# Kernel optimization log

Hardware: AMD Instinct MI355X
Metric: run time of the kernel (lower is better)

## Reference

```python
import jax, jax.numpy as jnp
import numpy as np

MARGIN = 0.3
FAMILY_TABLE = jnp.array([0, 1, 2, 1, 3, 3], dtype=jnp.int32)  # num_classes == 6
_BIG = 1e9  # finite sentinel (avoids inf*0 NaNs under autodiff)
_EPS = 1e-12  # F.normalize eps


def setup_inputs() -> dict:
    key = jax.random.key(0)
    k1, k2 = jax.random.split(key)
    B, D = 8192, 64
    embeddings = jax.random.normal(k1, (B, D), dtype=jnp.float32)
    labels = jax.random.randint(k2, (B,), 0, 6, dtype=jnp.int64)
    return {"embeddings": embeddings, "labels": labels}


def reference(embeddings, labels):
    B = embeddings.shape[0]
    # fam[i] = family_table[labels[i]]; labels are always < len(table) here,
    # so no -1 entries occur (matches original semantics for in-range labels).
    fam = jnp.take(FAMILY_TABLE, labels)  # [B]

    # L2-normalize rows (F.normalize with eps clamp)
    norm = jnp.maximum(jnp.linalg.norm(embeddings, axis=-1, keepdims=True), _EPS)
    emb_norm = embeddings / norm

    # cosine distance matrix [B, B]
    dist = 1.0 - emb_norm @ emb_norm.T

    same = (fam[:, None] == fam[None, :]) & (~jnp.eye(B, dtype=bool))  # [B,B]
    diff = fam[:, None] != fam[None, :]                                 # [B,B]

    d_pos = jnp.max(jnp.where(same, dist, -_BIG), axis=1)  # hardest positive
    d_neg = jnp.min(jnp.where(diff, dist, _BIG), axis=1)   # hardest negative

    valid = same.any(axis=1) & diff.any(axis=1)  # rows contributing to loss
    per_row = jnp.where(valid, jax.nn.relu(d_pos - d_neg + MARGIN), 0.0)

    count = jnp.sum(valid.astype(jnp.float32))
    return jnp.sum(per_row) / jnp.maximum(count, 1.0)
```

## Files before the change

### kernel.cpp

```cpp
#include <hip/hip_runtime.h>
#include <math.h>

#define MARGIN 0.3f
#define NJ 32
#define NPAIR 8

typedef short bf16x8 __attribute__((ext_vector_type(8)));
typedef float f32x4 __attribute__((ext_vector_type(4)));
typedef unsigned int u32;
typedef const __attribute__((address_space(1))) u32* gp_t;
typedef __attribute__((address_space(3))) u32* lp_t;

__device__ __forceinline__ unsigned short f2bf_rne(float x) {
    unsigned b = __float_as_uint(x);
    unsigned r = b + 0x7FFFu + ((b >> 16) & 1u);
    return (unsigned short)(r >> 16);
}
__device__ __forceinline__ int fam_of(int lbl) { return (0xF64 >> (2 * lbl)) & 3; }

__global__ __launch_bounds__(1024) void sort_kernel(const int* __restrict__ labels,
                                                    int* __restrict__ posOf,
                                                    unsigned char* __restrict__ famSorted,
                                                    int* __restrict__ famLoHi,
                                                    unsigned* __restrict__ counter, int B) {
    const int t = threadIdx.x;
    const int lane = t & 63, w = t >> 6;
    if (t == 0) *counter = 0;
    int lc[4] = {0, 0, 0, 0};
    int lf[8], lr[8];
#pragma unroll
    for (int j = 0; j < 8; j++) {
        int f = fam_of(labels[t * 8 + j]);
        lf[j] = f; lr[j] = lc[f]++;
    }
    int inc[4];
#pragma unroll
    for (int f = 0; f < 4; f++) {
        int v = lc[f];
#pragma unroll
        for (int o = 1; o < 64; o <<= 1) {
            int u = __shfl_up(v, o, 64);
            if (lane >= o) v += u;
        }
        inc[f] = v;
    }
    __shared__ int waveTot[16][4], waveBase[16][4], famBase[4], famTotS[4];
    if (lane == 63)
#pragma unroll
        for (int f = 0; f < 4; f++) waveTot[w][f] = inc[f];
    __syncthreads();
    if (t < 64) {
        int f = t >> 4, ww = t & 15;
        int v = waveTot[ww][f];
#pragma unroll
        for (int o = 1; o < 16; o <<= 1) {
            int u = __shfl_up(v, o, 64);
            if ((t & 15) >= o) v += u;
        }
        waveBase[ww][f] = v - waveTot[ww][f];
        if (ww == 15) famTotS[f] = v;
    }
    __syncthreads();
    if (t == 0) {
        int b = 0;
#pragma unroll
        for (int f = 0; f < 4; f++) {
            famBase[f] = b; famLoHi[f] = b; b += famTotS[f]; famLoHi[4 + f] = b;
        }
    }
    __syncthreads();
    int base[4];
#pragma unroll
    for (int f = 0; f < 4; f++) base[f] = famBase[f] + waveBase[w][f] + (inc[f] - lc[f]);
#pragma unroll
    for (int j = 0; j < 8; j++) {
        int pos = base[lf[j]] + lr[j];
        posOf[t * 8 + j] = pos;
        famSorted[pos] = (unsigned char)lf[j];
    }
}

__global__ __launch_bounds__(256) void normpack_kernel(const float* __restrict__ emb,
                                                       const int* __restrict__ posOf,
                                                       short* __restrict__ pack, int B) {
    const int lane = threadIdx.x & 63;
    const int wid  = threadIdx.x >> 6;
    const int row  = blockIdx.x * 4 + wid;
    float x = emb[(size_t)row * 64 + lane];
    float ss = x * x;
#pragma unroll
    for (int o = 32; o > 0; o >>= 1) ss += __shfl_xor(ss, o, 64);
    float n = fmaxf(sqrtf(ss), 1e-12f);
    unsigned short h = f2bf_rne(x / n);
    int pos = posOf[row];
    size_t idx = (size_t)(pos >> 4) * 1024 + (size_t)(lane >> 3) * 128 + (size_t)(pos & 15) * 8 + (lane & 7);
    pack[idx] = (short)h;
}

__global__ __launch_bounds__(256) void gemm_minmax_kernel(
    const short* __restrict__ pack,
    const unsigned char* __restrict__ famSorted, const int* __restrict__ famLoHi,
    float* __restrict__ pMin, float* __restrict__ pMax, int B) {
    __shared__ short ldsB[16384];

    const int lane = threadIdx.x & 63;
    const int wid  = threadIdx.x >> 6;
    const int g = lane >> 4;
    const int c = lane & 15;
    const int rowBase = blockIdx.x * 256 + wid * 64;
    const int aStrip0 = rowBase >> 4;
    const int jChunk0 = blockIdx.y * 256;
    const int jStrip0 = jChunk0 >> 4;

    bf16x8 aH[4][2];
#pragma unroll
    for (int s = 0; s < 4; s++) {
        const short* pA = pack + (size_t)(aStrip0 + s) * 1024;
        aH[s][0] = *(const bf16x8*)(pA + lane * 8);
        aH[s][1] = *(const bf16x8*)(pA + 512 + lane * 8);
    }

    {
        const char* src = (const char*)(pack + (size_t)jStrip0 * 1024);
#pragma unroll
        for (int i = 0; i < 8; i++) {
            int off = wid * 8192 + i * 1024;
            __builtin_amdgcn_global_load_lds((gp_t)(src + off + lane * 16),
                                             (lp_t)((char*)ldsB + off), 16, 0, 0);
        }
    }

    int sLo[4], sHi[4], sUni[4];
#pragma unroll
    for (int s = 0; s < 4; s++) {
        int f0  = famSorted[rowBase + s * 16];
        int f15 = famSorted[rowBase + s * 16 + 15];
        sUni[s] = __builtin_amdgcn_readfirstlane((f0 == f15) ? 1 : 0);
        sLo[s]  = __builtin_amdgcn_readfirstlane(famLoHi[f0]);
        sHi[s]  = __builtin_amdgcn_readfirstlane(famLoHi[4 + f0]);
    }

    const f32x4 zq = {0.f, 0.f, 0.f, 0.f};
    float mn[4] = {1e30f, 1e30f, 1e30f, 1e30f};
    float mx[4] = {-1e30f, -1e30f, -1e30f, -1e30f};

    __syncthreads();

#pragma unroll
    for (int jp = 0; jp < NPAIR; jp++) {
        const int j0 = jChunk0 + jp * 32;
        const short* pB0 = ldsB + (size_t)(2 * jp) * 1024;
        const short* pB1 = pB0 + 1024;
        bf16x8 b0h0 = *(const bf16x8*)(pB0 + lane * 8);
        bf16x8 b0h1 = *(const bf16x8*)(pB0 + 512 + lane * 8);
        bf16x8 b1h0 = *(const bf16x8*)(pB1 + lane * 8);
        bf16x8 b1h1 = *(const bf16x8*)(pB1 + 512 + lane * 8);

#pragma unroll
        for (int s = 0; s < 4; s++) {
            f32x4 accA, accB;
            accA = __builtin_amdgcn_mfma_f32_16x16x32_bf16(b0h0, aH[s][0], zq, 0, 0, 0);
            accB = __builtin_amdgcn_mfma_f32_16x16x32_bf16(b1h0, aH[s][0], zq, 0, 0, 0);
            accA = __builtin_amdgcn_mfma_f32_16x16x32_bf16(b0h1, aH[s][1], accA, 0, 0, 0);
            accB = __builtin_amdgcn_mfma_f32_16x16x32_bf16(b1h1, aH[s][1], accB, 0, 0, 0);

            if (sUni[s] && j0 >= sLo[s] && j0 + 32 <= sHi[s]) {
                float a01 = fminf(accA[0], accA[1]), a23 = fminf(accA[2], accA[3]);
                float b01 = fminf(accB[0], accB[1]), b23 = fminf(accB[2], accB[3]);
                mn[s] = fminf(mn[s], fminf(fminf(a01, a23), fminf(b01, b23)));
            } else if (sUni[s] && (j0 >= sHi[s] || j0 + 32 <= sLo[s])) {
                float a01 = fmaxf(accA[0], accA[1]), a23 = fmaxf(accA[2], accA[3]);
                float b01 = fmaxf(accB[0], accB[1]), b23 = fmaxf(accB[2], accB[3]);
                mx[s] = fmaxf(mx[s], fmaxf(fmaxf(a01, a23), fmaxf(b01, b23)));
            } else {
                int fi = famSorted[rowBase + s * 16 + c];
                unsigned fjA = *(const unsigned*)(famSorted + j0 + g * 4);
                unsigned fjB = *(const unsigned*)(famSorted + j0 + 16 + g * 4);
#pragma unroll
                for (int r = 0; r < 4; r++) {
                    bool sameA = ((int)((fjA >> (8 * r)) & 255u) == fi);
                    bool sameB = ((int)((fjB >> (8 * r)) & 255u) == fi);
                    mn[s] = fminf(mn[s], sameA ? accA[r] : 1e30f);
                    mx[s] = fmaxf(mx[s], sameA ? -1e30f : accA[r]);
                    mn[s] = fminf(mn[s], sameB ? accB[r] : 1e30f);
                    mx[s] = fmaxf(mx[s], sameB ? -1e30f : accB[r]);
                }
            }
        }
    }

#pragma unroll
    for (int s = 0; s < 4; s++) {
        float mnv = mn[s], mxv = mx[s];
        mnv = fminf(mnv, __shfl_xor(mnv, 16, 64));
        mxv = fmaxf(mxv, __shfl_xor(mxv, 16, 64));
        mnv = fminf(mnv, __shfl_xor(mnv, 32, 64));
        mxv = fmaxf(mxv, __shfl_xor(mxv, 32, 64));
        if (g == 0) {
            int row = rowBase + s * 16 + c;
            pMin[(size_t)blockIdx.y * B + row] = mnv;
            pMax[(size_t)blockIdx.y * B + row] = mxv;
        }
    }
}

__global__ __launch_bounds__(256) void rowloss_final_kernel(const float* __restrict__ pMin,
                                                            const float* __restrict__ pMax,
                                                            float* __restrict__ partial,
                                                            unsigned* __restrict__ counter,
                                                            float* __restrict__ out, int B) {
    const int nb = B / 256;
    const int row = blockIdx.x * 256 + threadIdx.x;
    float mn = 1e30f, mx = -1e30f;
#pragma unroll 8
    for (int cn = 0; cn < NJ; cn++) {
        mn = fminf(mn, pMin[(size_t)cn * B + row]);
        mx = fmaxf(mx, pMax[(size_t)cn * B + row]);
    }
    float sum = 0.f, cnt = 0.f;
    if (mn < 1e29f && mx > -1e29f) {
        sum = fmaxf(mx - mn + MARGIN, 0.f);
        cnt = 1.f;
    }
#pragma unroll
    for (int o = 32; o > 0; o >>= 1) {
        sum += __shfl_xor(sum, o, 64);
        cnt += __shfl_xor(cnt, o, 64);
    }
    __shared__ float sS[4], sC[4];
    const int lane = threadIdx.x & 63, w = threadIdx.x >> 6;
    if (lane == 0) { sS[w] = sum; sC[w] = cnt; }
    __syncthreads();
    if (threadIdx.x == 0) {
        partial[blockIdx.x]      = sS[0] + sS[1] + sS[2] + sS[3];
        partial[64 + blockIdx.x] = sC[0] + sC[1] + sC[2] + sC[3];
        __threadfence();
        unsigned done = atomicAdd(counter, 1u);
        if (done == (unsigned)(nb - 1)) {
            __threadfence();
            float S = 0.f, C = 0.f;
            for (int i = 0; i < nb; i++) { S += partial[i]; C += partial[64 + i]; }
            out[0] = S / fmaxf(C, 1.f);
        }
    }
}

extern "C" void kernel_launch(void* const* d_in, const int* in_sizes, int n_in,
                              void* d_out, int out_size, void* d_ws, size_t ws_size,
                              hipStream_t stream) {
    const float* emb    = (const float*)d_in[0];
    const int*   labels = (const int*)d_in[1];
    const int B = in_sizes[1];

    char* base = (char*)d_ws;
    size_t off = 0;
    auto alloc = [&](size_t bytes) -> char* {
        char* p = base + off;
        off = (off + bytes + 255) & ~(size_t)255;
        return p;
    };
    int*           posOf     = (int*)alloc((size_t)B * 4);
    unsigned char* famSorted = (unsigned char*)alloc((size_t)B);
    int*           famLoHi   = (int*)alloc(32);
    unsigned*      counter   = (unsigned*)alloc(64);
    short*         pack      = (short*)alloc((size_t)B * 64 * 2);
    float*         pMin      = (float*)alloc((size_t)NJ * B * 4);
    float*         pMax      = (float*)alloc((size_t)NJ * B * 4);
    float*         partial   = (float*)alloc(128 * 4);

    sort_kernel<<<1, 1024, 0, stream>>>(labels, posOf, famSorted, famLoHi, counter, B);
    normpack_kernel<<<B / 4, 256, 0, stream>>>(emb, posOf, pack, B);
    dim3 g3(B / 256, NJ);
    gemm_minmax_kernel<<<g3, 256, 0, stream>>>(pack, famSorted, famLoHi, pMin, pMax, B);
    rowloss_final_kernel<<<B / 256, 256, 0, stream>>>(pMin, pMax, partial, counter,
                                                      (float*)d_out, B);
}
```

Measured before the change: 33.26 us.

## Switch to 32x32 MFMA tiles and fuse row-loss reduction into GEMM tail

Repacks normalized embeddings into 32-row strips so the GEMM can use 32x32x16 bf16 MFMA, with each wave covering 128 rows against 256 columns. The separate row-loss kernel is folded into the GEMM: the last 32 blocks to finish spin until all 512 blocks have written their partial min/max, then reduce rows and compute the final loss. This removes a kernel launch and uses larger MFMA tiles, at the cost of higher register pressure and a spin-wait that relies on every block being resident or finishing.

```diff
diff --git a/kernel.cpp b/kernel.cpp
--- a/kernel.cpp
+++ b/kernel.cpp
@@ -2,11 +2,9 @@
 #include <math.h>
 
 #define MARGIN 0.3f
-#define NJ 32
-#define NPAIR 8
 
 typedef short bf16x8 __attribute__((ext_vector_type(8)));
-typedef float f32x4 __attribute__((ext_vector_type(4)));
+typedef float f32x16 __attribute__((ext_vector_type(16)));
 typedef unsigned int u32;
 typedef const __attribute__((address_space(1))) u32* gp_t;
 typedef __attribute__((address_space(3))) u32* lp_t;
@@ -22,10 +20,10 @@
                                                     int* __restrict__ posOf,
                                                     unsigned char* __restrict__ famSorted,
                                                     int* __restrict__ famLoHi,
-                                                    unsigned* __restrict__ counter, int B) {
+                                                    unsigned* __restrict__ counters, int B) {
     const int t = threadIdx.x;
     const int lane = t & 63, w = t >> 6;
-    if (t == 0) *counter = 0;
+    if (t < 2) counters[t] = 0;
     int lc[4] = {0, 0, 0, 0};
     int lf[8], lr[8];
 #pragma unroll
@@ -93,35 +91,40 @@
     float n = fmaxf(sqrtf(ss), 1e-12f);
     unsigned short h = f2bf_rne(x / n);
     int pos = posOf[row];
-    size_t idx = (size_t)(pos >> 4) * 1024 + (size_t)(lane >> 3) * 128 + (size_t)(pos & 15) * 8 + (lane & 7);
+    size_t idx = (size_t)(pos >> 5) * 2048 + (size_t)(lane >> 4) * 512 +
+                 (size_t)((lane >> 3) & 1) * 256 + (size_t)(pos & 31) * 8 + (lane & 7);
     pack[idx] = (short)h;
 }
 
-__global__ __launch_bounds__(256) void gemm_minmax_kernel(
+__global__ __launch_bounds__(256, 2) void gemm_tail_kernel(
     const short* __restrict__ pack,
     const unsigned char* __restrict__ famSorted, const int* __restrict__ famLoHi,
-    float* __restrict__ pMin, float* __restrict__ pMax, int B) {
+    float* __restrict__ pMin, float* __restrict__ pMax,
+    unsigned* __restrict__ counters, float* __restrict__ partial,
+    float* __restrict__ out, int B) {
     __shared__ short ldsB[16384];
-
-    const int lane = threadIdx.x & 63;
-    const int wid  = threadIdx.x >> 6;
-    const int g = lane >> 4;
-    const int c = lane & 15;
-    const int rowBase = blockIdx.x * 256 + wid * 64;
-    const int aStrip0 = rowBase >> 4;
-    const int jChunk0 = blockIdx.y * 256;
-    const int jStrip0 = jChunk0 >> 4;
-
-    bf16x8 aH[4][2];
+    const int t    = threadIdx.x;
+    const int lane = t & 63;
+    const int wid  = t >> 6;
+    const int half = lane >> 5;
+    const int il   = lane & 31;
+    const int rowBlock = blockIdx.x & 15;
+    const int colBlock = blockIdx.x >> 4;
+    const int rowBase  = rowBlock * 512 + wid * 128;
+    const int aStrip0  = rowBase >> 5;
+    const int jChunk0  = colBlock * 256;
+    const int jStrip0  = jChunk0 >> 5;
+
+    bf16x8 aH[4][4];
 #pragma unroll
     for (int s = 0; s < 4; s++) {
-        const short* pA = pack + (size_t)(aStrip0 + s) * 1024;
-        aH[s][0] = *(const bf16x8*)(pA + lane * 8);
-        aH[s][1] = *(const bf16x8*)(pA + 512 + lane * 8);
-    }
-
+        const short* pA = pack + (size_t)(aStrip0 + s) * 2048;
+#pragma unroll
+        for (int kw = 0; kw < 4; kw++)
+            aH[s][kw] = *(const bf16x8*)(pA + kw * 512 + lane * 8);
+    }
     {
-        const char* src = (const char*)(pack + (size_t)jStrip0 * 1024);
+        const char* src = (const char*)(pack + (size_t)jStrip0 * 2048);
 #pragma unroll
         for (int i = 0; i < 8; i++) {
             int off = wid * 8192 + i * 1024;
@@ -129,57 +132,64 @@
                                              (lp_t)((char*)ldsB + off), 16, 0, 0);
         }
     }
-
     int sLo[4], sHi[4], sUni[4];
 #pragma unroll
     for (int s = 0; s < 4; s++) {
-        int f0  = famSorted[rowBase + s * 16];
-        int f15 = famSorted[rowBase + s * 16 + 15];
-        sUni[s] = __builtin_amdgcn_readfirstlane((f0 == f15) ? 1 : 0);
+        int f0  = famSorted[rowBase + s * 32];
+        int f31 = famSorted[rowBase + s * 32 + 31];
+        sUni[s] = __builtin_amdgcn_readfirstlane((f0 == f31) ? 1 : 0);
         sLo[s]  = __builtin_amdgcn_readfirstlane(famLoHi[f0]);
         sHi[s]  = __builtin_amdgcn_readfirstlane(famLoHi[4 + f0]);
     }
-
-    const f32x4 zq = {0.f, 0.f, 0.f, 0.f};
+    const f32x16 zq = {0.f};
     float mn[4] = {1e30f, 1e30f, 1e30f, 1e30f};
     float mx[4] = {-1e30f, -1e30f, -1e30f, -1e30f};
 
     __syncthreads();
 
 #pragma unroll
-    for (int jp = 0; jp < NPAIR; jp++) {
-        const int j0 = jChunk0 + jp * 32;
-        const short* pB0 = ldsB + (size_t)(2 * jp) * 1024;
-        const short* pB1 = pB0 + 1024;
-        bf16x8 b0h0 = *(const bf16x8*)(pB0 + lane * 8);
-        bf16x8 b0h1 = *(const bf16x8*)(pB0 + 512 + lane * 8);
-        bf16x8 b1h0 = *(const bf16x8*)(pB1 + lane * 8);
-        bf16x8 b1h1 = *(const bf16x8*)(pB1 + 512 + lane * 8);
-
+    for (int pr = 0; pr < 4; pr++) {
+        const int j0 = jChunk0 + pr * 64;
+        const short* pB0 = ldsB + pr * 4096;
+        const short* pB1 = pB0 + 2048;
+        bf16x8 bA[4], bB[4];
+#pragma unroll
+        for (int kw = 0; kw < 4; kw++) {
+            bA[kw] = *(const bf16x8*)(pB0 + kw * 512 + lane * 8);
+            bB[kw] = *(const bf16x8*)(pB1 + kw * 512 + lane * 8);
+        }
 #pragma unroll
         for (int s = 0; s < 4; s++) {
-            f32x4 accA, accB;
-            accA = __builtin_amdgcn_mfma_f32_16x16x32_bf16(b0h0, aH[s][0], zq, 0, 0, 0);
-            accB = __builtin_amdgcn_mfma_f32_16x16x32_bf16(b1h0, aH[s][0], zq, 0, 0, 0);
-            accA = __builtin_amdgcn_mfma_f32_16x16x32_bf16(b0h1, aH[s][1], accA, 0, 0, 0);
-            accB = __builtin_amdgcn_mfma_f32_16x16x32_bf16(b1h1, aH[s][1], accB, 0, 0, 0);
-
-            if (sUni[s] && j0 >= sLo[s] && j0 + 32 <= sHi[s]) {
-                float a01 = fminf(accA[0], accA[1]), a23 = fminf(accA[2], accA[3]);
-                float b01 = fminf(accB[0], accB[1]), b23 = fminf(accB[2], accB[3]);
-                mn[s] = fminf(mn[s], fminf(fminf(a01, a23), fminf(b01, b23)));
-            } else if (sUni[s] && (j0 >= sHi[s] || j0 + 32 <= sLo[s])) {
-                float a01 = fmaxf(accA[0], accA[1]), a23 = fmaxf(accA[2], accA[3]);
-                float b01 = fmaxf(accB[0], accB[1]), b23 = fmaxf(accB[2], accB[3]);
-                mx[s] = fmaxf(mx[s], fmaxf(fmaxf(a01, a23), fmaxf(b01, b23)));
+            f32x16 accA = __builtin_amdgcn_mfma_f32_32x32x16_bf16(bA[0], aH[s][0], zq, 0, 0, 0);
+            f32x16 accB = __builtin_amdgcn_mfma_f32_32x32x16_bf16(bB[0], aH[s][0], zq, 0, 0, 0);
+            accA = __builtin_amdgcn_mfma_f32_32x32x16_bf16(bA[1], aH[s][1], accA, 0, 0, 0);
+            accB = __builtin_amdgcn_mfma_f32_32x32x16_bf16(bB[1], aH[s][1], accB, 0, 0, 0);
+            accA = __builtin_amdgcn_mfma_f32_32x32x16_bf16(bA[2], aH[s][2], accA, 0, 0, 0);
+            accB = __builtin_amdgcn_mfma_f32_32x32x16_bf16(bB[2], aH[s][2], accB, 0, 0, 0);
+            accA = __builtin_amdgcn_mfma_f32_32x32x16_bf16(bA[3], aH[s][3], accA, 0, 0, 0);
+            accB = __builtin_amdgcn_mfma_f32_32x32x16_bf16(bB[3], aH[s][3], accB, 0, 0, 0);
+
+            if (sUni[s] && j0 >= sLo[s] && j0 + 64 <= sHi[s]) {
+#pragma unroll
+                for (int r = 0; r < 16; r++)
+                    mn[s] = fminf(fminf(mn[s], accA[r]), accB[r]);
+            } else if (sUni[s] && (j0 >= sHi[s] || j0 + 64 <= sLo[s])) {
+#pragma unroll
+                for (int r = 0; r < 16; r++)
+                    mx[s] = fmaxf(fmaxf(mx[s], accA[r]), accB[r]);
             } else {
-                int fi = famSorted[rowBase + s * 16 + c];
-                unsigned fjA = *(const unsigned*)(famSorted + j0 + g * 4);
-                unsigned fjB = *(const unsigned*)(famSorted + j0 + 16 + g * 4);
-#pragma unroll
-                for (int r = 0; r < 4; r++) {
-                    bool sameA = ((int)((fjA >> (8 * r)) & 255u) == fi);
-                    bool sameB = ((int)((fjB >> (8 * r)) & 255u) == fi);
+                int fi = famSorted[rowBase + s * 32 + il];
+                u32 wA[4], wB[4];
+#pragma unroll
+                for (int q = 0; q < 4; q++) {
+                    wA[q] = *(const u32*)(famSorted + j0 + q * 8 + 4 * half);
+                    wB[q] = *(const u32*)(famSorted + j0 + 32 + q * 8 + 4 * half);
+                }
+#pragma unroll
+                for (int r = 0; r < 16; r++) {
+                    int fjA = (int)((wA[r >> 2] >> ((r & 3) * 8)) & 255u);
+                    int fjB = (int)((wB[r >> 2] >> ((r & 3) * 8)) & 255u);
+                    bool sameA = (fjA == fi), sameB = (fjB == fi);
                     mn[s] = fminf(mn[s], sameA ? accA[r] : 1e30f);
                     mx[s] = fmaxf(mx[s], sameA ? -1e30f : accA[r]);
                     mn[s] = fminf(mn[s], sameB ? accB[r] : 1e30f);
@@ -191,56 +201,56 @@
 
 #pragma unroll
     for (int s = 0; s < 4; s++) {
-        float mnv = mn[s], mxv = mx[s];
-        mnv = fminf(mnv, __shfl_xor(mnv, 16, 64));
-        mxv = fmaxf(mxv, __shfl_xor(mxv, 16, 64));
-        mnv = fminf(mnv, __shfl_xor(mnv, 32, 64));
-        mxv = fmaxf(mxv, __shfl_xor(mxv, 32, 64));
-        if (g == 0) {
-            int row = rowBase + s * 16 + c;
-            pMin[(size_t)blockIdx.y * B + row] = mnv;
-            pMax[(size_t)blockIdx.y * B + row] = mxv;
-        }
-    }
-}
-
-__global__ __launch_bounds__(256) void rowloss_final_kernel(const float* __restrict__ pMin,
-                                                            const float* __restrict__ pMax,
-                                                            float* __restrict__ partial,
-                                                            unsigned* __restrict__ counter,
-                                                            float* __restrict__ out, int B) {
-    const int nb = B / 256;
-    const int row = blockIdx.x * 256 + threadIdx.x;
-    float mn = 1e30f, mx = -1e30f;
+        float mnv = fminf(mn[s], __shfl_xor(mn[s], 32, 64));
+        float mxv = fmaxf(mx[s], __shfl_xor(mx[s], 32, 64));
+        if (half == 0) {
+            int row = rowBase + s * 32 + il;
+            pMin[(size_t)colBlock * B + row] = mnv;
+            pMax[(size_t)colBlock * B + row] = mxv;
+        }
+    }
+
+    __threadfence();
+    __shared__ unsigned sDone;
+    if (t == 0) sDone = atomicAdd(&counters[0], 1u);
+    __syncthreads();
+    unsigned done = sDone;
+    if (done >= 480u) {
+        if (t == 0) { while (atomicAdd(&counters[0], 0u) < 512u) {} }
+        __syncthreads();
+        __threadfence();
+        int slice = (int)done - 480;
+        int row = slice * 256 + t;
+        float rmn = 1e30f, rmx = -1e30f;
 #pragma unroll 8
-    for (int cn = 0; cn < NJ; cn++) {
-        mn = fminf(mn, pMin[(size_t)cn * B + row]);
-        mx = fmaxf(mx, pMax[(size_t)cn * B + row]);
-    }
-    float sum = 0.f, cnt = 0.f;
-    if (mn < 1e29f && mx > -1e29f) {
-        sum = fmaxf(mx - mn + MARGIN, 0.f);
-        cnt = 1.f;
-    }
-#pragma unroll
-    for (int o = 32; o > 0; o >>= 1) {
-        sum += __shfl_xor(sum, o, 64);
-        cnt += __shfl_xor(cnt, o, 64);
-    }
-    __shared__ float sS[4], sC[4];
-    const int lane = threadIdx.x & 63, w = threadIdx.x >> 6;
-    if (lane == 0) { sS[w] = sum; sC[w] = cnt; }
-    __syncthreads();
-    if (threadIdx.x == 0) {
-        partial[blockIdx.x]      = sS[0] + sS[1] + sS[2] + sS[3];
-        partial[64 + blockIdx.x] = sC[0] + sC[1] + sC[2] + sC[3];
-        __threadfence();
-        unsigned done = atomicAdd(counter, 1u);
-        if (done == (unsigned)(nb - 1)) {
+        for (int cn = 0; cn < 32; cn++) {
+            rmn = fminf(rmn, pMin[(size_t)cn * B + row]);
+            rmx = fmaxf(rmx, pMax[(size_t)cn * B + row]);
+        }
+        float sum = 0.f, cnt = 0.f;
+        if (rmn < 1e29f && rmx > -1e29f) {
+            sum = fmaxf(rmx - rmn + MARGIN, 0.f);
+            cnt = 1.f;
+        }
+#pragma unroll
+        for (int o = 32; o > 0; o >>= 1) {
+            sum += __shfl_xor(sum, o, 64);
+            cnt += __shfl_xor(cnt, o, 64);
+        }
+        __shared__ float sS[4], sC[4];
+        if (lane == 0) { sS[wid] = sum; sC[wid] = cnt; }
+        __syncthreads();
+        if (t == 0) {
+            partial[slice]      = sS[0] + sS[1] + sS[2] + sS[3];
+            partial[64 + slice] = sC[0] + sC[1] + sC[2] + sC[3];
             __threadfence();
-            float S = 0.f, C = 0.f;
-            for (int i = 0; i < nb; i++) { S += partial[i]; C += partial[64 + i]; }
-            out[0] = S / fmaxf(C, 1.f);
+            unsigned d2 = atomicAdd(&counters[1], 1u);
+            if (d2 == 31u) {
+                __threadfence();
+                float S = 0.f, C = 0.f;
+                for (int i = 0; i < 32; i++) { S += partial[i]; C += partial[64 + i]; }
+                out[0] = S / fmaxf(C, 1.f);
+            }
         }
     }
 }
@@ -261,17 +271,15 @@
     };
     int*           posOf     = (int*)alloc((size_t)B * 4);
     unsigned char* famSorted = (unsigned char*)alloc((size_t)B);
-    int*           famLoHi   = (int*)alloc(32);
-    unsigned*      counter   = (unsigned*)alloc(64);
+    int*           famLoHi   = (int*)alloc(64);
+    unsigned*      counters  = (unsigned*)alloc(64);
     short*         pack      = (short*)alloc((size_t)B * 64 * 2);
-    float*         pMin      = (float*)alloc((size_t)NJ * B * 4);
-    float*         pMax      = (float*)alloc((size_t)NJ * B * 4);
+    float*         pMin      = (float*)alloc((size_t)32 * B * 4);
+    float*         pMax      = (float*)alloc((size_t)32 * B * 4);
     float*         partial   = (float*)alloc(128 * 4);
 
-    sort_kernel<<<1, 1024, 0, stream>>>(labels, posOf, famSorted, famLoHi, counter, B);
+    sort_kernel<<<1, 1024, 0, stream>>>(labels, posOf, famSorted, famLoHi, counters, B);
     normpack_kernel<<<B / 4, 256, 0, stream>>>(emb, posOf, pack, B);
-    dim3 g3(B / 256, NJ);
-    gemm_minmax_kernel<<<g3, 256, 0, stream>>>(pack, famSorted, famLoHi, pMin, pMax, B);
-    rowloss_final_kernel<<<B / 256, 256, 0, stream>>>(pMin, pMax, partial, counter,
-                                                      (float*)d_out, B);
-}
+    gemm_tail_kernel<<<512, 256, 0, stream>>>(pack, famSorted, famLoHi, pMin, pMax,
+                                              counters, partial, (float*)d_out, B);
+}
```

Measured after the change: 78.41 us. 136% more time.
